# Kernel tuning notes

Measured on AMD Instinct MI355X. Metric: run time of the kernel, lower is better.

The kernel has to match this reference:

```python
import jax, jax.numpy as jnp
import numpy as np

V, D, NL, S, B = 32000, 1024, 2, 2048, 1
EXPAND, N, K = 2, 16, 4
DI = EXPAND * D
EPS = 1e-5


def setup_inputs() -> dict:
    key = jax.random.key(0)
    ks = jax.random.split(key, 10)
    std = 0.02
    inp = {
        "input_ids": jax.random.randint(ks[0], (B, S), 0, V),
        "embedding": jax.random.normal(ks[1], (V, D), jnp.float32) * std,
        "in_proj_w": jax.random.normal(ks[2], (NL, 2 * DI, D), jnp.float32) * std,
        "conv_w": jax.random.normal(ks[3], (NL, DI, 1, K), jnp.float32) * std,
        "conv_b": jnp.zeros((NL, DI), jnp.float32),
        "x_proj_w": jax.random.normal(ks[4], (NL, 2 * N, DI), jnp.float32) * std,
        "dt_proj_w": jax.random.normal(ks[5], (NL, DI, DI), jnp.float32) * std,
        "dt_proj_b": jnp.zeros((NL, DI), jnp.float32),
        "A_log": jnp.broadcast_to(jnp.log(jnp.arange(1, N + 1, dtype=jnp.float32)), (NL, DI, N)).copy(),
        "D_param": jnp.ones((NL, DI), jnp.float32),
        "out_proj_w": jax.random.normal(ks[6], (NL, D, DI), jnp.float32) * std,
        "norm_w": jnp.ones((NL, D), jnp.float32),
        "norm_f_w": jnp.ones((D,), jnp.float32),
        "lm_head_w": jax.random.normal(ks[7], (V, D), jnp.float32) * std,
    }
    return inp


def rmsnorm(x, w):
    rms = jnp.sqrt(jnp.mean(x * x, axis=-1, keepdims=True) + EPS)
    return x / rms * w


def silu(x):
    return x * jax.nn.sigmoid(x)


def ssm_layer(x, in_w, cw, cb, xp_w, dt_w, dt_b, A_log, Dp):
    b, s, _ = x.shape
    xz = jnp.einsum("bsd,ed->bse", x, in_w)  # (B,S,2*DI)
    xi, z = jnp.split(xz, 2, axis=-1)
    # depthwise causal conv1d
    xc = jnp.swapaxes(xi, 1, 2)  # (B,DI,S)
    xc = jax.lax.conv_general_dilated(
        xc, cw, window_strides=(1,), padding=[(K - 1, 0)],
        dimension_numbers=("NCH", "OIH", "NCH"), feature_group_count=DI,
    ) + cb[None, :, None]
    xi = silu(jnp.swapaxes(xc, 1, 2))  # (B,S,DI)
    bc = jnp.einsum("bsd,ed->bse", xi, xp_w)  # (B,S,2N)
    Bc, Cc = jnp.split(bc, 2, axis=-1)
    dt = jax.nn.softplus(jnp.einsum("bsd,ed->bse", xi, dt_w) + dt_b)
    A = -jnp.exp(A_log)  # (DI,N)
    dA = jnp.exp(dt[..., None] * A)                      # (B,S,DI,N)
    dBu = dt[..., None] * Bc[:, :, None, :] * xi[..., None]  # (B,S,DI,N)

    def step(h, t):
        dA_t, dBu_t, C_t, u_t = t
        h = dA_t * h + dBu_t                     # (B,DI,N)
        y = jnp.sum(h * C_t[:, None, :], axis=-1) + Dp * u_t  # (B,DI)
        return h, y

    xs = (jnp.swapaxes(dA, 0, 1), jnp.swapaxes(dBu, 0, 1),
          jnp.swapaxes(Cc, 0, 1), jnp.swapaxes(xi, 0, 1))
    h0 = jnp.zeros((b, DI, N), x.dtype)
    _, ys = jax.lax.scan(step, h0, xs)
    y = jnp.swapaxes(ys, 0, 1)  # (B,S,DI)
    y = y * silu(z)
    return y


def reference(input_ids, embedding, in_proj_w, conv_w, conv_b, x_proj_w,
              dt_proj_w, dt_proj_b, A_log, D_param, out_proj_w, norm_w,
              norm_f_w, lm_head_w):
    x = embedding[input_ids]  # (B,S,D)
    for l in range(NL):
        h = rmsnorm(x, norm_w[l])
        y = ssm_layer(h, in_proj_w[l], conv_w[l], conv_b[l], x_proj_w[l],
                      dt_proj_w[l], dt_proj_b[l], A_log[l], D_param[l])
        x = x + jnp.einsum("bse,de->bsd", y, out_proj_w[l])
    x = rmsnorm(x, norm_f_w)
    logits = jnp.einsum("bsd,vd->bsv", x, lm_head_w)
    return logits
```

## Files before the change

### kernel.cpp

```cpp
#include <hip/hip_runtime.h>
#include <hip/hip_bf16.h>
#include <stdint.h>
#include <stddef.h>

#define Vv   32000
#define Dd   1024
#define NLay 2
#define Ss   2048
#define Nn   16
#define Kc   4
#define DIc  2048
#define EPSf 1e-5f
#define LCH  32
#define NCHc (Ss / LCH)
#define CATR 2176

typedef __attribute__((ext_vector_type(8))) short bf16x8;
typedef __attribute__((ext_vector_type(4))) short s16x4;
typedef __attribute__((ext_vector_type(4))) float f32x4;

__device__ __forceinline__ short f2bf(float f) {
  union { float f; unsigned u; } a; a.f = f;
  return (short)((a.u + 0x7FFFu + ((a.u >> 16) & 1u)) >> 16);
}
__device__ __forceinline__ float bf2f(short s) {
  union { unsigned u; float f; } a; a.u = ((unsigned)(unsigned short)s) << 16;
  return a.f;
}
__device__ __forceinline__ int hswz(int r) { return (r & 3) ^ ((r >> 2) & 3); }

struct CvtSeg { const float* s; short* d; unsigned n4; };
struct CvtBatch { CvtSeg seg[7]; unsigned tot4; };
__global__ __launch_bounds__(256) void cvt_all_k(CvtBatch b) {
  for (unsigned idx = blockIdx.x * 256 + threadIdx.x; idx < b.tot4;
       idx += gridDim.x * 256) {
    unsigned r = idx;
    int sg = 0;
    while (sg < 6 && r >= b.seg[sg].n4) { r -= b.seg[sg].n4; ++sg; }
    float4 v = ((const float4*)b.seg[sg].s)[r];
    s16x4 o;
    o.x = f2bf(v.x); o.y = f2bf(v.y); o.z = f2bf(v.z); o.w = f2bf(v.w);
    __builtin_nontemporal_store(o, &((s16x4*)b.seg[sg].d)[r]);
  }
}

__global__ __launch_bounds__(256) void embed_norm_k(const int* __restrict__ ids,
                                                    const float* __restrict__ emb,
                                                    const float* __restrict__ w,
                                                    float* __restrict__ x,
                                                    short* __restrict__ o) {
  int s = blockIdx.x, t = threadIdx.x;
  int id = ids[s];
  float4 v = ((const float4*)(emb + (size_t)id * Dd))[t];
  ((float4*)(x + (size_t)s * Dd))[t] = v;
  float ss = v.x * v.x + v.y * v.y + v.z * v.z + v.w * v.w;
#pragma unroll
  for (int off = 32; off; off >>= 1) ss += __shfl_down(ss, off);
  __shared__ float red[4];
  if ((t & 63) == 0) red[t >> 6] = ss;
  __syncthreads();
  ss = red[0] + red[1] + red[2] + red[3];
  float rinv = rsqrtf(ss * (1.0f / Dd) + EPSf);
  float4 wv = ((const float4*)w)[t];
  short4 ov;
  ov.x = f2bf(v.x * rinv * wv.x);
  ov.y = f2bf(v.y * rinv * wv.y);
  ov.z = f2bf(v.z * rinv * wv.z);
  ov.w = f2bf(v.w * rinv * wv.w);
  ((short4*)(o + (size_t)s * Dd))[t] = ov;
}

__global__ __launch_bounds__(256) void rmsnorm_k(const float* __restrict__ x,
                                                 const float* __restrict__ w,
                                                 short* __restrict__ o) {
  int s = blockIdx.x, t = threadIdx.x;
  float4 v = ((const float4*)(x + (size_t)s * Dd))[t];
  float ss = v.x * v.x + v.y * v.y + v.z * v.z + v.w * v.w;
#pragma unroll
  for (int off = 32; off; off >>= 1) ss += __shfl_down(ss, off);
  __shared__ float red[4];
  if ((t & 63) == 0) red[t >> 6] = ss;
  __syncthreads();
  ss = red[0] + red[1] + red[2] + red[3];
  float rinv = rsqrtf(ss * (1.0f / Dd) + EPSf);
  float4 wv = ((const float4*)w)[t];
  short4 ov;
  ov.x = f2bf(v.x * rinv * wv.x);
  ov.y = f2bf(v.y * rinv * wv.y);
  ov.z = f2bf(v.z * rinv * wv.z);
  ov.w = f2bf(v.w * rinv * wv.w);
  ((short4*)(o + (size_t)s * Dd))[t] = ov;
}

template <int BM, int BN, int WM, int WN, bool RESID, bool CAT, bool OBF16 = false>
__global__ __launch_bounds__(WM * WN * 64, 2) void gemm_ring(
    const short* __restrict__ A, const short* __restrict__ B,
    float* C, const float* resb, float* C2, int M, int N, int K, int nMt) {
  constexpr int NT = WM * WN * 64;
  constexpr int FM = BM / (WM * 16);
  constexpr int FN = BN / (WN * 16);
  constexpr int PA = BM * 4 / NT;
  constexpr int PB = BN * 4 / NT;
  static_assert(PA + PB == 4, "vmcnt literals assume 4 loads per stage");
  __shared__ short lds[4][(BM + BN) * 32];
  const int t = threadIdx.x;
  const int lane = t & 63;
  const int w = t >> 6;
  const int wm = w / WN, wn = w % WN;
  const int lr = lane & 15, l4 = lane >> 4;
  const int nwg = gridDim.x;
  const int chunk = nwg >> 3;
  const int wg = (blockIdx.x & 7) * chunk + (blockIdx.x >> 3);
  const int mi = wg % nMt, ni = wg / nMt;
  const size_t rowBase = (size_t)mi * BM, colBase = (size_t)ni * BN;

  const short* aSrc[PA]; int aOff[PA];
  const short* bSrc[PB]; int bOff[PB];
#pragma unroll
  for (int p = 0; p < PA; ++p) {
    int q = p * NT + t;
    int row = q >> 2, s = q & 3;
    aSrc[p] = A + (rowBase + row) * K + ((s ^ hswz(row)) << 3);
    aOff[p] = q * 8;
  }
#pragma unroll
  for (int p = 0; p < PB; ++p) {
    int q = p * NT + t;
    int row = q >> 2, s = q & 3;
    bSrc[p] = B + (colBase + row) * K + ((s ^ hswz(row)) << 3);
    bOff[p] = BM * 32 + q * 8;
  }
  auto stage = [&](int buf, int k0) {
#pragma unroll
    for (int p = 0; p < PA; ++p)
      __builtin_amdgcn_global_load_lds(
          (__attribute__((address_space(1))) unsigned int*)(aSrc[p] + k0),
          (__attribute__((address_space(3))) unsigned int*)(&lds[buf][aOff[p]]), 16, 0, 0);
#pragma unroll
    for (int p = 0; p < PB; ++p)
      __builtin_amdgcn_global_load_lds(
          (__attribute__((address_space(1))) unsigned int*)(bSrc[p] + k0),
          (__attribute__((address_space(3))) unsigned int*)(&lds[buf][bOff[p]]), 16, 0, 0);
  };

  f32x4 acc[FM][FN];
#pragma unroll
  for (int i = 0; i < FM; i++)
#pragma unroll
    for (int j = 0; j < FN; j++) acc[i][j] = f32x4{0.f, 0.f, 0.f, 0.f};

  const int KT = K >> 5;
  stage(0, 0); stage(1, 32); stage(2, 64);
  for (int kt = 0; kt < KT; ++kt) {
    const int rem = KT - 1 - kt;
    __builtin_amdgcn_sched_barrier(0);
    if (rem >= 2)      asm volatile("s_waitcnt vmcnt(8)" ::: "memory");
    else if (rem == 1) asm volatile("s_waitcnt vmcnt(4)" ::: "memory");
    else               asm volatile("s_waitcnt vmcnt(0)" ::: "memory");
    __builtin_amdgcn_sched_barrier(0);
    __builtin_amdgcn_s_barrier();
    __builtin_amdgcn_sched_barrier(0);
    if (kt + 3 < KT) stage((kt + 3) & 3, (kt + 3) << 5);
    const short* la = &lds[kt & 3][0];
    const short* lb = &lds[kt & 3][BM * 32];
    bf16x8 av[FM], bv[FN];
#pragma unroll
    for (int i = 0; i < FM; i++) {
      int r = wm * (FM * 16) + i * 16 + lr;
      av[i] = *(const bf16x8*)&la[r * 32 + ((l4 ^ hswz(r)) << 3)];
    }
#pragma unroll
    for (int j = 0; j < FN; j++) {
      int r = wn * (FN * 16) + j * 16 + lr;
      bv[j] = *(const bf16x8*)&lb[r * 32 + ((l4 ^ hswz(r)) << 3)];
    }
    __builtin_amdgcn_s_setprio(1);
#pragma unroll
    for (int i = 0; i < FM; i++)
#pragma unroll
      for (int j = 0; j < FN; j++)
        acc[i][j] = __builtin_amdgcn_mfma_f32_16x16x32_bf16(av[i], bv[j], acc[i][j], 0, 0, 0);
    __builtin_amdgcn_s_setprio(0);
  }
#pragma unroll
  for (int i = 0; i < FM; i++) {
#pragma unroll
    for (int j = 0; j < FN; j++) {
      size_t r0 = rowBase + wm * (FM * 16) + i * 16 + l4 * 4;
      size_t c = colBase + wn * (FN * 16) + j * 16 + lr;
#pragma unroll
      for (int rr = 0; rr < 4; rr++) {
        size_t r = r0 + rr;
        float v = acc[i][j][rr];
        if (CAT) {
          if (c < DIc) {
            float xv = v + resb[c];
            C[r * DIc + c] = fmaxf(xv, 0.f) + log1pf(__expf(-fabsf(xv)));
          } else if (c < DIc + 2 * Nn) {
            C2[r * (2 * Nn) + (c - DIc)] = v;
          }
        } else if (OBF16) {
          ((short*)C)[r * N + c] = f2bf(v);
        } else {
          size_t idx = r * N + c;
          if (RESID) v += resb[idx];
          C[idx] = v;
        }
      }
    }
  }
}

__global__ __launch_bounds__(512, 2) void gemm256(const short* __restrict__ A,
                                                  const short* __restrict__ B,
                                                  float* __restrict__ C,
                                                  int M, int N, int K, int nMt) {
  __shared__ short lds[2][2][256 * 64];
  const int t = threadIdx.x;
  const int lane = t & 63;
  const int w = t >> 6;
  const int wm = w >> 2, wn = w & 3;
  const int lr = lane & 15, l4 = lane >> 4;
  const int nwg = gridDim.x;
  const int chunk = nwg >> 3;
  const int wg = (blockIdx.x & 7) * chunk + (blockIdx.x >> 3);
  const int mi = wg % nMt, ni = wg / nMt;
  const size_t rowBase = (size_t)mi * 256, colBase = (size_t)ni * 256;

  const short* aSrc[4]; const short* bSrc[4];
  int ldsOff[4];
#pragma unroll
  for (int p = 0; p < 4; ++p) {
    int q = p * 512 + t;
    int row = q >> 3, s = q & 7;
    int ks = (s ^ (row & 7)) * 8;
    aSrc[p] = A + (rowBase + row) * K + ks;
    bSrc[p] = B + (colBase + row) * K + ks;
    ldsOff[p] = q * 8;
  }
  auto stage = [&](int buf, int k0) {
#pragma unroll
    for (int p = 0; p < 4; ++p)
      __builtin_amdgcn_global_load_lds(
          (__attribute__((address_space(1))) unsigned int*)(aSrc[p] + k0),
          (__attribute__((address_space(3))) unsigned int*)(&lds[buf][0][ldsOff[p]]), 16, 0, 0);
#pragma unroll
    for (int p = 0; p < 4; ++p)
      __builtin_amdgcn_global_load_lds(
          (__attribute__((address_space(1))) unsigned int*)(bSrc[p] + k0),
          (__attribute__((address_space(3))) unsigned int*)(&lds[buf][1][ldsOff[p]]), 16, 0, 0);
  };

  f32x4 acc[8][4];
#pragma unroll
  for (int i = 0; i < 8; i++)
#pragma unroll
    for (int j = 0; j < 4; j++) acc[i][j] = f32x4{0.f, 0.f, 0.f, 0.f};

  stage(0, 0);
  const int KT = K >> 6;
  for (int kt = 0; kt < KT; ++kt) {
    const int cur = kt & 1;
    __syncthreads();
    bf16x8 a0[4][2], b0[4][2];
#pragma unroll
    for (int i = 0; i < 4; i++)
#pragma unroll
      for (int kq = 0; kq < 2; kq++) {
        int r = wm * 128 + i * 16 + lr;
        int ks = kq * 4 + l4;
        a0[i][kq] = *(const bf16x8*)&lds[cur][0][r * 64 + ((ks ^ (r & 7)) << 3)];
      }
#pragma unroll
    for (int j = 0; j < 4; j++)
#pragma unroll
      for (int kq = 0; kq < 2; kq++) {
        int r = wn * 64 + j * 16 + lr;
        int ks = kq * 4 + l4;
        b0[j][kq] = *(const bf16x8*)&lds[cur][1][r * 64 + ((ks ^ (r & 7)) << 3)];
      }
    if (kt + 1 < KT) stage(cur ^ 1, (kt + 1) << 6);
    __builtin_amdgcn_s_setprio(1);
#pragma unroll
    for (int i = 0; i < 4; i++)
#pragma unroll
      for (int j = 0; j < 4; j++)
#pragma unroll
        for (int kq = 0; kq < 2; kq++)
          acc[i][j] = __builtin_amdgcn_mfma_f32_16x16x32_bf16(a0[i][kq], b0[j][kq], acc[i][j], 0, 0, 0);
    __builtin_amdgcn_s_setprio(0);
    bf16x8 a1[4][2];
#pragma unroll
    for (int i = 0; i < 4; i++)
#pragma unroll
      for (int kq = 0; kq < 2; kq++) {
        int r = wm * 128 + 64 + i * 16 + lr;
        int ks = kq * 4 + l4;
        a1[i][kq] = *(const bf16x8*)&lds[cur][0][r * 64 + ((ks ^ (r & 7)) << 3)];
      }
    __builtin_amdgcn_s_setprio(1);
#pragma unroll
    for (int i = 0; i < 4; i++)
#pragma unroll
      for (int j = 0; j < 4; j++)
#pragma unroll
        for (int kq = 0; kq < 2; kq++)
          acc[i + 4][j] = __builtin_amdgcn_mfma_f32_16x16x32_bf16(a1[i][kq], b0[j][kq], acc[i + 4][j], 0, 0, 0);
    __builtin_amdgcn_s_setprio(0);
  }
#pragma unroll
  for (int i = 0; i < 8; i++) {
#pragma unroll
    for (int j = 0; j < 4; j++) {
      size_t r0 = rowBase + wm * 128 + i * 16 + l4 * 4;
      size_t c = colBase + wn * 64 + j * 16 + lr;
#pragma unroll
      for (int rr = 0; rr < 4; rr++)
        C[(r0 + rr) * N + c] = acc[i][j][rr];
    }
  }
}

__global__ __launch_bounds__(256) void conv_silu_k(const short* __restrict__ xz,
                                                   const float* __restrict__ cw,
                                                   const float* __restrict__ cb,
                                                   short* __restrict__ xiC) {
  int idx = blockIdx.x * 256 + threadIdx.x;
  int s = idx / (DIc / 4), c4 = idx - s * (DIc / 4);
  const short4* xz4 = (const short4*)xz;
  const size_t rstride = 2 * DIc / 4;
  short4 zero = {0, 0, 0, 0};
  short4 x0 = (s >= 3) ? xz4[(size_t)(s - 3) * rstride + c4] : zero;
  short4 x1 = (s >= 2) ? xz4[(size_t)(s - 2) * rstride + c4] : zero;
  short4 x2 = (s >= 1) ? xz4[(size_t)(s - 1) * rstride + c4] : zero;
  short4 x3 = xz4[(size_t)s * rstride + c4];
  float4 cbv = ((const float4*)cb)[c4];
  float xs[4][4] = {{bf2f(x0.x), bf2f(x1.x), bf2f(x2.x), bf2f(x3.x)},
                    {bf2f(x0.y), bf2f(x1.y), bf2f(x2.y), bf2f(x3.y)},
                    {bf2f(x0.z), bf2f(x1.z), bf2f(x2.z), bf2f(x3.z)},
                    {bf2f(x0.w), bf2f(x1.w), bf2f(x2.w), bf2f(x3.w)}};
  float cbs[4] = {cbv.x, cbv.y, cbv.z, cbv.w};
  short os[4];
#pragma unroll
  for (int j = 0; j < 4; j++) {
    float4 wv = ((const float4*)cw)[c4 * 4 + j];
    float acc = cbs[j] + wv.x * xs[j][0] + wv.y * xs[j][1] + wv.z * xs[j][2] + wv.w * xs[j][3];
    os[j] = f2bf(acc / (1.f + __expf(-acc)));
  }
  short4 ov;
  ov.x = os[0]; ov.y = os[1]; ov.z = os[2]; ov.w = os[3];
  ((short4*)xiC)[idx] = ov;
}

__global__ __launch_bounds__(256) void scan_pass1(const float* __restrict__ dt,
                                                  const short* __restrict__ u,
                                                  const float* __restrict__ bc,
                                                  const float* __restrict__ alog,
                                                  float* __restrict__ Ap,
                                                  float* __restrict__ Hl) {
  const int j = blockIdx.x;
  const int d = blockIdx.y * 256 + threadIdx.x;
  __shared__ float sB[LCH][Nn];
  for (int q = threadIdx.x; q < LCH * Nn; q += 256) {
    int tt = q >> 4, n = q & 15;
    sB[tt][n] = bc[(size_t)(j * LCH + tt) * 32 + n];
  }
  __syncthreads();
  float Ar[Nn], h[Nn], ap[Nn];
#pragma unroll
  for (int n = 0; n < Nn; n++) {
    Ar[n] = -__expf(alog[d * Nn + n]); h[n] = 0.f; ap[n] = 1.f;
  }
  const int t0 = j * LCH;
  for (int tt = 0; tt < LCH; tt++) {
    size_t gi = (size_t)(t0 + tt) * DIc + d;
    float dtv = dt[gi];
    float uv = bf2f(u[gi]);
    float dtu = dtv * uv;
#pragma unroll
    for (int n = 0; n < Nn; n++) {
      float a = __expf(dtv * Ar[n]);
      h[n] = a * h[n] + dtu * sB[tt][n];
      ap[n] *= a;
    }
  }
  size_t base = ((size_t)j * DIc + d) * Nn;
#pragma unroll
  for (int n = 0; n < Nn; n++) { Ap[base + n] = ap[n]; Hl[base + n] = h[n]; }
}

__global__ __launch_bounds__(256) void scan_combine(const float* __restrict__ Ap,
                                                    const float* __restrict__ Hl,
                                                    float* __restrict__ Hi) {
  int idx = blockIdx.x * 256 + threadIdx.x;
  float h = 0.f;
  for (int j0 = 0; j0 < NCHc; j0 += 8) {
    float ap[8], hl[8];
#pragma unroll
    for (int u = 0; u < 8; ++u) {
      size_t o = (size_t)(j0 + u) * DIc * Nn + idx;
      ap[u] = Ap[o]; hl[u] = Hl[o];
    }
#pragma unroll
    for (int u = 0; u < 8; ++u) {
      size_t o = (size_t)(j0 + u) * DIc * Nn + idx;
      Hi[o] = h;
      h = ap[u] * h + hl[u];
    }
  }
}

__global__ __launch_bounds__(256) void scan_pass2(const float* __restrict__ dt,
                                                  const short* __restrict__ u,
                                                  const float* __restrict__ bc,
                                                  const float* __restrict__ alog,
                                                  const float* __restrict__ Hinit,
                                                  const float* __restrict__ Dp,
                                                  const short* __restrict__ xz,
                                                  short* __restrict__ y) {
  const int j = blockIdx.x;
  const int d = blockIdx.y * 256 + threadIdx.x;
  __shared__ float sB[LCH][Nn], sC[LCH][Nn];
  for (int q = threadIdx.x; q < LCH * Nn; q += 256) {
    int tt = q >> 4, n = q & 15;
    size_t r = (size_t)(j * LCH + tt) * 32;
    sB[tt][n] = bc[r + n];
    sC[tt][n] = bc[r + 16 + n];
  }
  __syncthreads();
  float Ar[Nn], h[Nn];
  size_t hb = ((size_t)j * DIc + d) * Nn;
#pragma unroll
  for (int n = 0; n < Nn; n++) {
    Ar[n] = -__expf(alog[d * Nn + n]); h[n] = Hinit[hb + n];
  }
  float dp = Dp[d];
  const int t0 = j * LCH;
  for (int tt = 0; tt < LCH; tt++) {
    size_t gi = (size_t)(t0 + tt) * DIc + d;
    float dtv = dt[gi];
    float uv = bf2f(u[gi]);
    float dtu = dtv * uv;
    float yv = dp * uv;
#pragma unroll
    for (int n = 0; n < Nn; n++) {
      float a = __expf(dtv * Ar[n]);
      h[n] = a * h[n] + dtu * sB[tt][n];
      yv += h[n] * sC[tt][n];
    }
    float zv = bf2f(xz[(size_t)(t0 + tt) * (2 * DIc) + DIc + d]);
    float sz = zv / (1.f + __expf(-zv));
    y[gi] = f2bf(yv * sz);
  }
}

extern "C" void kernel_launch(void* const* d_in, const int* in_sizes, int n_in,
                              void* d_out, int out_size, void* d_ws, size_t ws_size,
                              hipStream_t stream) {
  (void)in_sizes; (void)n_in; (void)out_size; (void)ws_size;
  const int* ids = (const int*)d_in[0];
  const float* emb = (const float*)d_in[1];
  const float* in_proj_w = (const float*)d_in[2];
  const float* conv_w = (const float*)d_in[3];
  const float* conv_b = (const float*)d_in[4];
  const float* x_proj_w = (const float*)d_in[5];
  const float* dt_proj_w = (const float*)d_in[6];
  const float* dt_proj_b = (const float*)d_in[7];
  const float* A_log = (const float*)d_in[8];
  const float* D_param = (const float*)d_in[9];
  const float* out_proj_w = (const float*)d_in[10];
  const float* norm_w = (const float*)d_in[11];
  const float* norm_f_w = (const float*)d_in[12];
  const float* lm_head_w = (const float*)d_in[13];
  float* logits = (float*)d_out;

  char* ws = (char*)d_ws;
  size_t woff = 0;
  auto walloc = [&](size_t bytes) { void* p = ws + woff; woff += (bytes + 255) & ~(size_t)255; return p; };
  float* x     = (float*)walloc((size_t)Ss * Dd * 4);
  short* xfbf  = (short*)walloc((size_t)Ss * Dd * 2);
  short* w_lm  = (short*)walloc((size_t)Vv * Dd * 2);

  char* sc = (char*)d_out;
  size_t soff = 0;
  auto salloc = [&](size_t bytes) { void* p = sc + soff; soff += (bytes + 255) & ~(size_t)255; return p; };
  short* xz   = (short*)salloc((size_t)Ss * 2 * DIc * 2);
  float* dtb  = (float*)salloc((size_t)Ss * DIc * 4);
  float* bc   = (float*)salloc((size_t)Ss * 32 * 4);
  float* Ap   = (float*)salloc((size_t)NCHc * DIc * Nn * 4);
  float* Hl   = (float*)salloc((size_t)NCHc * DIc * Nn * 4);
  float* Hi   = (float*)salloc((size_t)NCHc * DIc * Nn * 4);
  short* hbf  = (short*)salloc((size_t)Ss * Dd * 2);
  short* xiC  = (short*)salloc((size_t)Ss * DIc * 2);
  short* ybf  = (short*)salloc((size_t)Ss * DIc * 2);
  short* w_in = (short*)salloc((size_t)NLay * 2 * DIc * Dd * 2);
  short* w_cat= (short*)salloc((size_t)NLay * CATR * DIc * 2);
  short* w_out= (short*)salloc((size_t)NLay * Dd * DIc * 2);

  CvtBatch cb2{};
  unsigned tot = 0;
  auto addseg = [&](int i, const float* s, short* d, size_t n) {
    cb2.seg[i].s = s; cb2.seg[i].d = d; cb2.seg[i].n4 = (unsigned)(n / 4);
    tot += (unsigned)(n / 4);
  };
  addseg(0, in_proj_w, w_in, (size_t)NLay * 2 * DIc * Dd);
  addseg(1, out_proj_w, w_out, (size_t)NLay * Dd * DIc);
  addseg(2, lm_head_w, w_lm, (size_t)Vv * Dd);
  addseg(3, dt_proj_w, w_cat, (size_t)DIc * DIc);
  addseg(4, x_proj_w, w_cat + (size_t)DIc * DIc, (size_t)2 * Nn * DIc);
  addseg(5, dt_proj_w + (size_t)DIc * DIc, w_cat + (size_t)CATR * DIc, (size_t)DIc * DIc);
  addseg(6, x_proj_w + (size_t)2 * Nn * DIc,
         w_cat + (size_t)CATR * DIc + (size_t)DIc * DIc, (size_t)2 * Nn * DIc);
  cb2.tot4 = tot;
  cvt_all_k<<<dim3(4096), dim3(256), 0, stream>>>(cb2);

  embed_norm_k<<<dim3(Ss), dim3(256), 0, stream>>>(ids, emb, norm_w, x, hbf);

  for (int l = 0; l < NLay; l++) {
    if (l > 0)
      rmsnorm_k<<<dim3(Ss), dim3(256), 0, stream>>>(x, norm_w + (size_t)l * Dd, hbf);
    gemm_ring<128, 128, 2, 2, false, false, true><<<dim3(512), dim3(256), 0, stream>>>(
        hbf, w_in + (size_t)l * 2 * DIc * Dd, (float*)xz, nullptr, nullptr, Ss, 2 * DIc, Dd, 16);
    conv_silu_k<<<dim3(Ss * DIc / 4 / 256), dim3(256), 0, stream>>>(
        xz, conv_w + (size_t)l * DIc * Kc, conv_b + (size_t)l * DIc, xiC);
    gemm_ring<128, 128, 2, 2, false, true><<<dim3(272), dim3(256), 0, stream>>>(
        xiC, w_cat + (size_t)l * CATR * DIc, dtb, dt_proj_b + (size_t)l * DIc, bc,
        Ss, CATR, DIc, 16);
    scan_pass1<<<dim3(NCHc, DIc / 256), dim3(256), 0, stream>>>(
        dtb, xiC, bc, A_log + (size_t)l * DIc * Nn, Ap, Hl);
    scan_combine<<<dim3(DIc * Nn / 256), dim3(256), 0, stream>>>(Ap, Hl, Hi);
    scan_pass2<<<dim3(NCHc, DIc / 256), dim3(256), 0, stream>>>(
        dtb, xiC, bc, A_log + (size_t)l * DIc * Nn, Hi,
        D_param + (size_t)l * DIc, xz, ybf);
    gemm_ring<128, 128, 2, 2, true, false><<<dim3(128), dim3(256), 0, stream>>>(
        ybf, w_out + (size_t)l * Dd * DIc, x, x, nullptr, Ss, Dd, DIc, 16);
  }

  rmsnorm_k<<<dim3(Ss), dim3(256), 0, stream>>>(x, norm_f_w, xfbf);
  gemm256<<<dim3(1000), dim3(512), 0, stream>>>(xfbf, w_lm, logits, Ss, Vv, Dd, 8);
}
```

Baseline: 647.0 us.

## Add 128x256 BK64 GEMM kernel for in_proj and fused dt/x_proj

Adds a new 512-thread GEMM with 128x256 tiles, BK=64, double-buffered LDS via direct global-to-LDS loads, and XOR-swizzled layout. It is used for the in_proj GEMM and the concatenated dt_proj/x_proj GEMM, whose row count is padded from 2176 to 2304 to fit 256-wide tiles. The goal is more data reuse per tile and fewer K iterations. The trade-offs are one workgroup per CU, fewer blocks (256 and 144), wasted padded columns, and dropping the nontemporal stores in weight conversion.

```diff
diff --git a/kernel.cpp b/kernel.cpp
--- a/kernel.cpp
+++ b/kernel.cpp
@@ -13,10 +13,9 @@
 #define EPSf 1e-5f
 #define LCH  32
 #define NCHc (Ss / LCH)
-#define CATR 2176
+#define CATR 2304
 
 typedef __attribute__((ext_vector_type(8))) short bf16x8;
-typedef __attribute__((ext_vector_type(4))) short s16x4;
 typedef __attribute__((ext_vector_type(4))) float f32x4;
 
 __device__ __forceinline__ short f2bf(float f) {
@@ -38,9 +37,9 @@
     int sg = 0;
     while (sg < 6 && r >= b.seg[sg].n4) { r -= b.seg[sg].n4; ++sg; }
     float4 v = ((const float4*)b.seg[sg].s)[r];
-    s16x4 o;
+    short4 o;
     o.x = f2bf(v.x); o.y = f2bf(v.y); o.z = f2bf(v.z); o.w = f2bf(v.w);
-    __builtin_nontemporal_store(o, &((s16x4*)b.seg[sg].d)[r]);
+    ((short4*)b.seg[sg].d)[r] = o;
   }
 }
 
@@ -92,10 +91,10 @@
   ((short4*)(o + (size_t)s * Dd))[t] = ov;
 }
 
-template <int BM, int BN, int WM, int WN, bool RESID, bool CAT, bool OBF16 = false>
+template <int BM, int BN, int WM, int WN, bool RESID>
 __global__ __launch_bounds__(WM * WN * 64, 2) void gemm_ring(
     const short* __restrict__ A, const short* __restrict__ B,
-    float* C, const float* resb, float* C2, int M, int N, int K, int nMt) {
+    float* C, const float* resb, int M, int N, int K, int nMt) {
   constexpr int NT = WM * WN * 64;
   constexpr int FM = BM / (WM * 16);
   constexpr int FN = BN / (WN * 16);
@@ -192,6 +191,108 @@
       for (int rr = 0; rr < 4; rr++) {
         size_t r = r0 + rr;
         float v = acc[i][j][rr];
+        size_t idx = r * N + c;
+        if (RESID) v += resb[idx];
+        C[idx] = v;
+      }
+    }
+  }
+}
+
+template <bool CAT, bool OBF16>
+__global__ __launch_bounds__(512, 1) void gemm_bk64(const short* __restrict__ A,
+                                                    const short* __restrict__ B,
+                                                    float* C, const float* __restrict__ resb,
+                                                    float* C2, int M, int N, int K, int nMt) {
+  __shared__ short lds[2][(128 + 256) * 64];
+  const int t = threadIdx.x;
+  const int lane = t & 63;
+  const int w = t >> 6;
+  const int wm = w >> 2, wn = w & 3;
+  const int lr = lane & 15, l4 = lane >> 4;
+  const int nwg = gridDim.x, chunk = nwg >> 3;
+  const int wg = (blockIdx.x & 7) * chunk + (blockIdx.x >> 3);
+  const int mi = wg % nMt, ni = wg / nMt;
+  const size_t rowBase = (size_t)mi * 128, colBase = (size_t)ni * 256;
+
+  const short* aSrc[2]; int aOff[2];
+  const short* bSrc[4]; int bOff[4];
+#pragma unroll
+  for (int p = 0; p < 2; ++p) {
+    int q = p * 512 + t;
+    int row = q >> 3, s = q & 7;
+    aSrc[p] = A + (rowBase + row) * (size_t)K + ((s ^ (row & 7)) << 3);
+    aOff[p] = q * 8;
+  }
+#pragma unroll
+  for (int p = 0; p < 4; ++p) {
+    int q = p * 512 + t;
+    int row = q >> 3, s = q & 7;
+    bSrc[p] = B + (colBase + row) * (size_t)K + ((s ^ (row & 7)) << 3);
+    bOff[p] = 128 * 64 + q * 8;
+  }
+  auto stage = [&](int buf, int k0) {
+#pragma unroll
+    for (int p = 0; p < 2; ++p)
+      __builtin_amdgcn_global_load_lds(
+          (__attribute__((address_space(1))) unsigned int*)(aSrc[p] + k0),
+          (__attribute__((address_space(3))) unsigned int*)(&lds[buf][aOff[p]]), 16, 0, 0);
+#pragma unroll
+    for (int p = 0; p < 4; ++p)
+      __builtin_amdgcn_global_load_lds(
+          (__attribute__((address_space(1))) unsigned int*)(bSrc[p] + k0),
+          (__attribute__((address_space(3))) unsigned int*)(&lds[buf][bOff[p]]), 16, 0, 0);
+  };
+
+  f32x4 acc[4][4];
+#pragma unroll
+  for (int i = 0; i < 4; i++)
+#pragma unroll
+    for (int j = 0; j < 4; j++) acc[i][j] = f32x4{0.f, 0.f, 0.f, 0.f};
+
+  stage(0, 0);
+  const int KT = K >> 6;
+  for (int kt = 0; kt < KT; ++kt) {
+    const int cur = kt & 1;
+    __syncthreads();
+    bf16x8 a0[4][2], b0[4][2];
+#pragma unroll
+    for (int i = 0; i < 4; i++)
+#pragma unroll
+      for (int kq = 0; kq < 2; kq++) {
+        int r = wm * 64 + i * 16 + lr;
+        int ks = kq * 4 + l4;
+        a0[i][kq] = *(const bf16x8*)&lds[cur][r * 64 + ((ks ^ (r & 7)) << 3)];
+      }
+#pragma unroll
+    for (int j = 0; j < 4; j++)
+#pragma unroll
+      for (int kq = 0; kq < 2; kq++) {
+        int r = wn * 64 + j * 16 + lr;
+        int ks = kq * 4 + l4;
+        b0[j][kq] = *(const bf16x8*)&lds[cur][128 * 64 + r * 64 + ((ks ^ (r & 7)) << 3)];
+      }
+    if (kt + 1 < KT) stage(cur ^ 1, (kt + 1) << 6);
+    __builtin_amdgcn_s_setprio(1);
+#pragma unroll
+    for (int i = 0; i < 4; i++)
+#pragma unroll
+      for (int j = 0; j < 4; j++)
+#pragma unroll
+        for (int kq = 0; kq < 2; kq++)
+          acc[i][j] = __builtin_amdgcn_mfma_f32_16x16x32_bf16(a0[i][kq], b0[j][kq], acc[i][j], 0, 0, 0);
+    __builtin_amdgcn_s_setprio(0);
+  }
+#pragma unroll
+  for (int i = 0; i < 4; i++) {
+#pragma unroll
+    for (int j = 0; j < 4; j++) {
+      size_t r0 = rowBase + wm * 64 + i * 16 + l4 * 4;
+      size_t c = colBase + wn * 64 + j * 16 + lr;
+#pragma unroll
+      for (int rr = 0; rr < 4; rr++) {
+        size_t r = r0 + rr;
+        float v = acc[i][j][rr];
         if (CAT) {
           if (c < DIc) {
             float xv = v + resb[c];
@@ -202,9 +303,7 @@
         } else if (OBF16) {
           ((short*)C)[r * N + c] = f2bf(v);
         } else {
-          size_t idx = r * N + c;
-          if (RESID) v += resb[idx];
-          C[idx] = v;
+          C[r * N + c] = v;
         }
       }
     }
@@ -519,11 +618,12 @@
   for (int l = 0; l < NLay; l++) {
     if (l > 0)
       rmsnorm_k<<<dim3(Ss), dim3(256), 0, stream>>>(x, norm_w + (size_t)l * Dd, hbf);
-    gemm_ring<128, 128, 2, 2, false, false, true><<<dim3(512), dim3(256), 0, stream>>>(
-        hbf, w_in + (size_t)l * 2 * DIc * Dd, (float*)xz, nullptr, nullptr, Ss, 2 * DIc, Dd, 16);
+    gemm_bk64<false, true><<<dim3(256), dim3(512), 0, stream>>>(
+        hbf, w_in + (size_t)l * 2 * DIc * Dd, (float*)xz, nullptr, nullptr,
+        Ss, 2 * DIc, Dd, 16);
     conv_silu_k<<<dim3(Ss * DIc / 4 / 256), dim3(256), 0, stream>>>(
         xz, conv_w + (size_t)l * DIc * Kc, conv_b + (size_t)l * DIc, xiC);
-    gemm_ring<128, 128, 2, 2, false, true><<<dim3(272), dim3(256), 0, stream>>>(
+    gemm_bk64<true, false><<<dim3(144), dim3(512), 0, stream>>>(
         xiC, w_cat + (size_t)l * CATR * DIc, dtb, dt_proj_b + (size_t)l * DIc, bc,
         Ss, CATR, DIc, 16);
     scan_pass1<<<dim3(NCHc, DIc / 256), dim3(256), 0, stream>>>(
@@ -532,8 +632,8 @@
     scan_pass2<<<dim3(NCHc, DIc / 256), dim3(256), 0, stream>>>(
         dtb, xiC, bc, A_log + (size_t)l * DIc * Nn, Hi,
         D_param + (size_t)l * DIc, xz, ybf);
-    gemm_ring<128, 128, 2, 2, true, false><<<dim3(128), dim3(256), 0, stream>>>(
-        ybf, w_out + (size_t)l * Dd * DIc, x, x, nullptr, Ss, Dd, DIc, 16);
+    gemm_ring<128, 128, 2, 2, true><<<dim3(128), dim3(256), 0, stream>>>(
+        ybf, w_out + (size_t)l * Dd * DIc, x, x, Ss, Dd, DIc, 16);
   }
 
   rmsnorm_k<<<dim3(Ss), dim3(256), 0, stream>>>(x, norm_f_w, xfbf);
```

After: 651.7 us. No clear change (+0.7%).
